# Performance work log

Hardware: AMD Instinct MI355X
Metric: run time of the kernel (lower is better)

The kernel has to match this reference:

```python
import jax, jax.numpy as jnp
import numpy as np

HID = 4096
HEADS = 32
HEAD_DIM = 128
SEQ = 2048
GROUP = 128          # AWQ quantization group size along the input (K) dim
QKV_OUT = 3 * HID
ROPE_BASE = 10000.0


def dequant(qweight, scales, zeros):
    # qweight: [K, N] int; scales/zeros: [K//GROUP, N]
    s = jnp.repeat(scales, GROUP, axis=0)
    z = jnp.repeat(zeros, GROUP, axis=0)
    return (qweight.astype(jnp.float32) - z) * s


def rotate_half(x):
    x1, x2 = jnp.split(x, 2, axis=-1)
    return jnp.concatenate((-x2, x1), axis=-1)


def setup_inputs() -> dict:
    key = jax.random.key(0)
    ks = jax.random.split(key, 8)
    hidden_states = jax.random.normal(ks[0], (1, SEQ, HID), dtype=jnp.float32)
    position_ids = jnp.arange(SEQ, dtype=jnp.int32)[None, :]
    qkv_qweight = jax.random.randint(ks[1], (HID, QKV_OUT), 0, 16, dtype=jnp.int32)
    qkv_scales = jax.random.uniform(ks[2], (HID // GROUP, QKV_OUT), dtype=jnp.float32) * 0.002
    qkv_zeros = jax.random.uniform(ks[3], (HID // GROUP, QKV_OUT), dtype=jnp.float32) * 16.0
    o_qweight = jax.random.randint(ks[4], (HID, HID), 0, 16, dtype=jnp.int32)
    o_scales = jax.random.uniform(ks[5], (HID // GROUP, HID), dtype=jnp.float32) * 0.002
    o_zeros = jax.random.uniform(ks[6], (HID // GROUP, HID), dtype=jnp.float32) * 16.0
    return {"hidden_states": hidden_states, "position_ids": position_ids,
            "qkv_qweight": qkv_qweight, "qkv_scales": qkv_scales, "qkv_zeros": qkv_zeros,
            "o_qweight": o_qweight, "o_scales": o_scales, "o_zeros": o_zeros}


def reference(hidden_states, position_ids, qkv_qweight, qkv_scales, qkv_zeros,
              o_qweight, o_scales, o_zeros):
    b, s, _ = hidden_states.shape
    # --- quantized QKV projection (dequant + GEMM) ---
    w_qkv = dequant(qkv_qweight, qkv_scales, qkv_zeros)        # [HID, 3*HID]
    proj = jnp.einsum('bsk,kn->bsn', hidden_states, w_qkv)     # [b, s, 3*HID]
    xqkv = proj.reshape(b, s, 3, HEADS, HEAD_DIM)
    # [b, h, s, d]
    q = jnp.transpose(xqkv[:, :, 0], (0, 2, 1, 3))
    k = jnp.transpose(xqkv[:, :, 1], (0, 2, 1, 3))
    v = jnp.transpose(xqkv[:, :, 2], (0, 2, 1, 3))
    # --- rotary embedding (no KV cache: kv_seq_len == s) ---
    inv_freq = 1.0 / (ROPE_BASE ** (jnp.arange(0, HEAD_DIM, 2, dtype=jnp.float32) / HEAD_DIM))
    t = jnp.arange(s, dtype=jnp.float32)
    freqs = jnp.outer(t, inv_freq)                             # [s, d/2]
    emb = jnp.concatenate((freqs, freqs), axis=-1)             # [s, d]
    cos = jnp.cos(emb)[position_ids][:, None]                  # [b, 1, s, d]
    sin = jnp.sin(emb)[position_ids][:, None]
    q = q * cos + rotate_half(q) * sin
    k = k * cos + rotate_half(k) * sin
    # --- causal attention (flash_attn_func, padding_mask=None branch) ---
    scale = 1.0 / jnp.sqrt(jnp.float32(HEAD_DIM))
    scores = jnp.einsum('bhqd,bhkd->bhqk', q, k) * scale       # [b, h, s, s]
    causal = jnp.tril(jnp.ones((s, s), dtype=bool))
    scores = jnp.where(causal, scores, jnp.float32(-1e30))
    probs = jax.nn.softmax(scores, axis=-1)
    attn = jnp.einsum('bhqk,bhkd->bhqd', probs, v)             # [b, h, s, d]
    attn = jnp.transpose(attn, (0, 2, 1, 3)).reshape(b, s, HID)
    # --- quantized output projection ---
    w_o = dequant(o_qweight, o_scales, o_zeros)                # [HID, HID]
    out = jnp.einsum('bsk,kn->bsn', attn, w_o)                 # [b, s, HID]
    return out
```

## Files before the change

### kernel.cpp

```cpp
#include <hip/hip_runtime.h>
#include <hip/hip_bf16.h>

#define S_LEN 2048
#define HID_DIM 4096
#define NH 32
#define HD 128
#define NQKV 12288

typedef _Float16 half2v __attribute__((ext_vector_type(2)));
typedef _Float16 half4v __attribute__((ext_vector_type(4)));
typedef _Float16 half8v __attribute__((ext_vector_type(8)));
typedef float f32x4 __attribute__((ext_vector_type(4)));

typedef const __attribute__((address_space(1))) unsigned int* gas_u32;
typedef __attribute__((address_space(3))) unsigned int* las_u32;

__device__ inline void g2lds16(const _Float16* g, _Float16* l) {
  __builtin_amdgcn_global_load_lds((gas_u32)g, (las_u32)l, 16, 0, 0);
}

__global__ __launch_bounds__(256) void dequant_w(const int* __restrict__ W,
                                                 const float* __restrict__ scal,
                                                 const float* __restrict__ zer,
                                                 _Float16* __restrict__ Wt, int K, int N) {
  __shared__ _Float16 lT[64 * 84];
  const int k0 = blockIdx.y * 64, n0 = blockIdx.x * 64;
  const int tid = threadIdx.x, c = tid & 63, rp = tid >> 6;
  const int g = k0 >> 7;
  const float sc = scal[(size_t)g * N + n0 + c];
  const float zp = zer[(size_t)g * N + n0 + c];
#pragma unroll
  for (int i = 0; i < 8; ++i) {
    const int k = i * 8 + rp * 2;
    const float q0 = (float)W[(size_t)(k0 + k) * N + n0 + c];
    const float q1 = (float)W[(size_t)(k0 + k + 1) * N + n0 + c];
    half2v p;
    p[0] = (_Float16)((q0 - zp) * sc);
    p[1] = (_Float16)((q1 - zp) * sc);
    *(half2v*)&lT[c * 84 + k] = p;
  }
  __syncthreads();
  const int kc = tid & 7, nr0 = tid >> 3;
#pragma unroll
  for (int i = 0; i < 2; ++i) {
    const int n = nr0 + 32 * i;
    union { half8v v8; half4v v4[2]; } u;
    u.v4[0] = *(const half4v*)&lT[n * 84 + kc * 8];
    u.v4[1] = *(const half4v*)&lT[n * 84 + kc * 8 + 4];
    *(half8v*)&Wt[(size_t)(n0 + n) * K + k0 + kc * 8] = u.v8;
  }
}

__global__ __launch_bounds__(256) void conv_a(const float* __restrict__ A, _Float16* __restrict__ Af) {
  const int i = blockIdx.x * 256 + threadIdx.x;
  const float4 t = ((const float4*)A)[i];
  half4v r;
  r[0] = (_Float16)t.x; r[1] = (_Float16)t.y; r[2] = (_Float16)t.z; r[3] = (_Float16)t.w;
  ((half4v*)Af)[i] = r;
}

__device__ inline void stage128x64(const _Float16* __restrict__ gp, int K,
                                   _Float16* lp, int wave, int stR, int stC) {
  g2lds16(gp + (size_t)(wave * 16 + stR) * K + stC, lp + (wave * 2) * 512);
  g2lds16(gp + (size_t)(wave * 16 + 8 + stR) * K + stC, lp + (wave * 2 + 1) * 512);
}
__device__ inline void stage64x64(const _Float16* __restrict__ gp, int K,
                                  _Float16* lp, int wave, int stR, int stC) {
  g2lds16(gp + (size_t)(wave * 8 + stR) * K + stC, lp + wave * 512);
}

template <int NBF, typename CT>
__global__ __launch_bounds__(512, 2) void gemm_2ph(const _Float16* __restrict__ A,
                                                   const _Float16* __restrict__ Bt,
                                                   CT* __restrict__ C, int M, int N, int K) {
  __shared__ _Float16 sA[3][2][128 * 64];
  __shared__ _Float16 sB[2][NBF * 64 * 64];

  const int tid = threadIdx.x;
  const int wave = tid >> 6, lane = tid & 63;
  const int quad = lane >> 4, l16 = lane & 15;
  const int wr = wave >> 2;
  const int wc = wave & 3;
  const int NT = K >> 6;

  const _Float16* Ab = A + (size_t)(blockIdx.y * 256) * K;
  const _Float16* Bb = Bt + (size_t)(blockIdx.x * (NBF * 64)) * K;

  const int stR = lane >> 3;
  const int stC = ((lane & 7) ^ stR) << 3;
  const int fx = l16 & 7;

#define COFF(ks_) ((((ks_) * 4 + quad) ^ fx) << 3)
#define SYNC_MFMA()                                  \
  __builtin_amdgcn_s_barrier();                      \
  asm volatile("s_waitcnt lgkmcnt(0)" ::: "memory"); \
  __builtin_amdgcn_sched_barrier(0);

  f32x4 acc[8][NBF];
  const f32x4 zero4 = {0.f, 0.f, 0.f, 0.f};
#pragma unroll
  for (int m8 = 0; m8 < 8; ++m8)
#pragma unroll
    for (int nb = 0; nb < NBF; ++nb) acc[m8][nb] = zero4;

#pragma unroll
  for (int j = 0; j < NBF; ++j)
    stage64x64(Bb + (size_t)(j * 64) * K, K, &sB[0][j * 4096], wave, stR, stC);
  stage128x64(Ab, K, &sA[0][0][0], wave, stR, stC);
  stage128x64(Ab + (size_t)128 * K, K, &sA[0][1][0], wave, stR, stC);
  stage128x64(Ab + 64, K, &sA[1][0][0], wave, stR, stC);
  stage128x64(Ab + (size_t)128 * K + 64, K, &sA[1][1][0], wave, stR, stC);
  asm volatile("s_waitcnt vmcnt(4)" ::: "memory");
  __builtin_amdgcn_s_barrier();

  int bA = 0;
  for (int t = 0; t < NT; ++t) {
    const int bB = t & 1;
    const int bA2 = (bA + 2 >= 3) ? bA - 1 : bA + 2;
    half8v af[4][2], bf[NBF][2];

#pragma unroll
    for (int mb = 0; mb < 4; ++mb)
#pragma unroll
      for (int ks = 0; ks < 2; ++ks)
        af[mb][ks] = *(const half8v*)&sA[bA][wr][(mb * 16 + l16) * 64 + COFF(ks)];
#pragma unroll
    for (int nb = 0; nb < NBF; ++nb)
#pragma unroll
      for (int ks = 0; ks < 2; ++ks)
        bf[nb][ks] = *(const half8v*)&sB[bB][(wc * (NBF * 16) + nb * 16 + l16) * 64 + COFF(ks)];
    if (t + 1 < NT) {
#pragma unroll
      for (int j = 0; j < NBF; ++j)
        stage64x64(Bb + (size_t)(j * 64) * K + (size_t)(t + 1) * 64, K,
                   &sB[bB ^ 1][j * 4096], wave, stR, stC);
    }
    SYNC_MFMA()
    __builtin_amdgcn_s_setprio(1);
#pragma unroll
    for (int mb = 0; mb < 4; ++mb)
#pragma unroll
      for (int nb = 0; nb < NBF; ++nb)
#pragma unroll
        for (int ks = 0; ks < 2; ++ks)
          acc[mb][nb] =
              __builtin_amdgcn_mfma_f32_16x16x32_f16(af[mb][ks], bf[nb][ks], acc[mb][nb], 0, 0, 0);
    __builtin_amdgcn_s_setprio(0);

#pragma unroll
    for (int mb = 0; mb < 4; ++mb)
#pragma unroll
      for (int ks = 0; ks < 2; ++ks)
        af[mb][ks] = *(const half8v*)&sA[bA][wr][(64 + mb * 16 + l16) * 64 + COFF(ks)];
    if (t + 2 < NT) {
      const _Float16* Ap = Ab + (size_t)(t + 2) * 64;
      stage128x64(Ap, K, &sA[bA2][0][0], wave, stR, stC);
      stage128x64(Ap + (size_t)128 * K, K, &sA[bA2][1][0], wave, stR, stC);
      asm volatile("s_waitcnt vmcnt(4)" ::: "memory");
    } else if (t + 1 < NT) {
      asm volatile("s_waitcnt vmcnt(0)" ::: "memory");
    }
    SYNC_MFMA()
    __builtin_amdgcn_s_setprio(1);
#pragma unroll
    for (int mb = 0; mb < 4; ++mb)
#pragma unroll
      for (int nb = 0; nb < NBF; ++nb)
#pragma unroll
        for (int ks = 0; ks < 2; ++ks)
          acc[4 + mb][nb] = __builtin_amdgcn_mfma_f32_16x16x32_f16(af[mb][ks], bf[nb][ks],
                                                                   acc[4 + mb][nb], 0, 0, 0);
    __builtin_amdgcn_s_setprio(0);

    bA = (bA + 1 >= 3) ? 0 : bA + 1;
  }

  const int rbase = blockIdx.y * 256 + wr * 128 + quad * 4;
  const int cbase = blockIdx.x * (NBF * 64) + wc * (NBF * 16) + l16;
#pragma unroll
  for (int m8 = 0; m8 < 8; ++m8) {
    const int rowb = rbase + (m8 >> 2) * 64 + (m8 & 3) * 16;
#pragma unroll
    for (int nb = 0; nb < NBF; ++nb)
#pragma unroll
      for (int i = 0; i < 4; ++i)
        C[(size_t)(rowb + i) * N + cbase + nb * 16] = (CT)acc[m8][nb][i];
  }
#undef COFF
#undef SYNC_MFMA
}

__global__ __launch_bounds__(256) void rope_kernel(const _Float16* __restrict__ proj,
                                                   const int* __restrict__ pos,
                                                   _Float16* __restrict__ Q, _Float16* __restrict__ K,
                                                   _Float16* __restrict__ Vt) {
  const int h = blockIdx.x, sb = blockIdx.y;
  const int tid = threadIdx.x;
  const int s0 = sb * 64;

#pragma unroll
  for (int it = 0; it < 16; ++it) {
    const int idx = it * 256 + tid;
    const int sl = idx >> 6, j = idx & 63;
    const int s = s0 + sl;
    const float p = (float)pos[s];
    const float invrev = exp2f(-0.20762050593045455f * (float)j) * 0.15915494309189535f;
    const float rev = p * invrev;
    const float frac = rev - floorf(rev);
    const float sn = __builtin_amdgcn_sinf(frac);
    const float cs = __builtin_amdgcn_cosf(frac);
    const _Float16* rp = proj + (size_t)s * NQKV + h * HD;
    {
      const float x1 = (float)rp[j], x2 = (float)rp[j + 64];
      _Float16* qp = Q + ((size_t)h * S_LEN + s) * HD;
      qp[j] = (_Float16)(x1 * cs - x2 * sn);
      qp[j + 64] = (_Float16)(x2 * cs + x1 * sn);
    }
    {
      const float x1 = (float)rp[HID_DIM + j], x2 = (float)rp[HID_DIM + j + 64];
      _Float16* kp = K + ((size_t)h * S_LEN + s) * HD;
      kp[j] = (_Float16)(x1 * cs - x2 * sn);
      kp[j + 64] = (_Float16)(x2 * cs + x1 * sn);
    }
  }

  __shared__ _Float16 lV[64 * 132];
#pragma unroll
  for (int r = 0; r < 4; ++r) {
    const int cid = r * 256 + tid;
    const int sl = cid >> 4;
    const int d0 = (cid & 15) * 8;
    const _Float16* vp = proj + (size_t)(s0 + sl) * NQKV + 2 * HID_DIM + h * HD + d0;
    *(half4v*)&lV[sl * 132 + d0] = *(const half4v*)vp;
    *(half4v*)&lV[sl * 132 + d0 + 4] = *(const half4v*)(vp + 4);
  }
  __syncthreads();
#pragma unroll
  for (int it = 0; it < 32; ++it) {
    const int d = it * 4 + (tid >> 6);
    const int sl = tid & 63;
    Vt[((size_t)h * HD + d) * S_LEN + s0 + sl] = lV[sl * 132 + d];
  }
}

__global__ __launch_bounds__(256) void flash_attn(const _Float16* __restrict__ Q,
                                                  const _Float16* __restrict__ Km,
                                                  const _Float16* __restrict__ Vt,
                                                  _Float16* __restrict__ O) {
  __shared__ _Float16 lK[4][32 * 128];
  __shared__ _Float16 lV[4][128 * 32];
  __shared__ _Float16 lP[4][2][16 * 40];
  const int h = blockIdx.y;
  const int xb = blockIdx.x;
  const int qb = (xb & 1) ? (15 - (xb >> 1)) : (xb >> 1);
  const int tid = threadIdx.x;
  const int wave = tid >> 6, lane = tid & 63;
  const int quad = lane >> 4, l16 = lane & 15;
  const int q0w = qb * 128 + wave * 32;
  const float scale = 0.08838834764831845f;

  const _Float16* Qh = Q + (size_t)h * S_LEN * HD;
  const _Float16* Kh = Km + (size_t)h * S_LEN * HD;
  const _Float16* Vh = Vt + (size_t)h * HD * S_LEN;

  const int kRow0 = wave * 8 + (lane >> 4);
  const int kSlot = lane & 15;
  const int vRow0 = wave * 32 + (lane >> 2);
  const int vSlot = lane & 3;

  auto stage_kv = [&](int kt_, int buf_) {
#pragma unroll
    for (int i = 0; i < 2; ++i) {
      const int row = kRow0 + i * 4;
      const int ck = kSlot ^ (row & 15);
      g2lds16(Kh + (size_t)(kt_ * 32 + row) * HD + ck * 8, &lK[buf_][(wave * 8 + i * 4) * 128]);
    }
#pragma unroll
    for (int i = 0; i < 2; ++i) {
      const int row = vRow0 + i * 16;
      const int cv = vSlot ^ ((row >> 1) & 3);
      g2lds16(Vh + (size_t)row * S_LEN + kt_ * 32 + cv * 8, &lV[buf_][(wave * 32 + i * 16) * 32]);
    }
  };

  half8v qf[2][4];
#pragma unroll
  for (int r = 0; r < 2; ++r)
#pragma unroll
    for (int c = 0; c < 4; ++c)
      qf[r][c] = *(const half8v*)&Qh[(size_t)(q0w + r * 16 + l16) * HD + c * 32 + quad * 8];

  const f32x4 zero4 = {0.f, 0.f, 0.f, 0.f};
  f32x4 o[2][8];
  f32x4 lp[2];
#pragma unroll
  for (int r = 0; r < 2; ++r) {
    lp[r] = zero4;
#pragma unroll
    for (int c = 0; c < 8; ++c) o[r][c] = zero4;
  }

  const int ntiles = 4 * qb + 4;
  stage_kv(0, 0);
  stage_kv(1, 1);

  for (int kt = 0; kt < ntiles; ++kt) {
    const int cb = kt & 3;
    if (kt + 2 < ntiles) {
      stage_kv(kt + 2, (kt + 2) & 3);
      asm volatile("s_waitcnt vmcnt(8)" ::: "memory");
    } else if (kt + 1 < ntiles) {
      asm volatile("s_waitcnt vmcnt(4)" ::: "memory");
    } else {
      asm volatile("s_waitcnt vmcnt(0)" ::: "memory");
    }
    __builtin_amdgcn_s_barrier();

    half8v kf[2][4];
#pragma unroll
    for (int hf = 0; hf < 2; ++hf)
#pragma unroll
      for (int c = 0; c < 4; ++c) {
        const int slot = (c * 4 + quad) ^ l16;
        kf[hf][c] = *(const half8v*)&lK[cb][(hf * 16 + l16) * 128 + slot * 8];
      }
    half8v vf[8];
#pragma unroll
    for (int c = 0; c < 8; ++c) {
      const int slot = quad ^ ((l16 >> 1) & 3);
      vf[c] = *(const half8v*)&lV[cb][(c * 16 + l16) * 32 + slot * 8];
    }

    f32x4 s[2][2];
#pragma unroll
    for (int r = 0; r < 2; ++r)
#pragma unroll
      for (int hf = 0; hf < 2; ++hf) {
        s[r][hf] = zero4;
#pragma unroll
        for (int c = 0; c < 4; ++c)
          s[r][hf] = __builtin_amdgcn_mfma_f32_16x16x32_f16(qf[r][c], kf[hf][c], s[r][hf], 0, 0, 0);
      }

#pragma unroll
    for (int r = 0; r < 2; ++r) {
      float p0[4], p1[4];
#pragma unroll
      for (int i = 0; i < 4; ++i) {
        const int row = q0w + r * 16 + quad * 4 + i;
        const int col0 = kt * 32 + l16, col1 = col0 + 16;
        const float e0 = __expf(s[r][0][i] * scale);
        const float e1 = __expf(s[r][1][i] * scale);
        p0[i] = (col0 <= row) ? e0 : 0.f;
        p1[i] = (col1 <= row) ? e1 : 0.f;
        lp[r][i] += p0[i] + p1[i];
      }
      _Float16* pw = lP[wave][r];
#pragma unroll
      for (int i = 0; i < 4; ++i) {
        pw[(quad * 4 + i) * 40 + l16] = (_Float16)p0[i];
        pw[(quad * 4 + i) * 40 + l16 + 16] = (_Float16)p1[i];
      }
    }
    half8v pa[2];
#pragma unroll
    for (int r = 0; r < 2; ++r) pa[r] = *(half8v*)&lP[wave][r][l16 * 40 + quad * 8];

#pragma unroll
    for (int c = 0; c < 8; ++c)
#pragma unroll
      for (int r = 0; r < 2; ++r)
        o[r][c] = __builtin_amdgcn_mfma_f32_16x16x32_f16(pa[r], vf[c], o[r][c], 0, 0, 0);
  }

#pragma unroll
  for (int r = 0; r < 2; ++r) {
    f32x4 ls = lp[r];
#pragma unroll
    for (int off = 1; off < 16; off <<= 1) {
#pragma unroll
      for (int i = 0; i < 4; ++i) ls[i] += __shfl_xor(ls[i], off);
    }
    f32x4 inv;
#pragma unroll
    for (int i = 0; i < 4; ++i) inv[i] = 1.f / ls[i];
#pragma unroll
    for (int c = 0; c < 8; ++c) {
#pragma unroll
      for (int i = 0; i < 4; ++i) {
        const int row = q0w + r * 16 + quad * 4 + i;
        O[(size_t)row * HID_DIM + h * HD + c * 16 + l16] = (_Float16)(o[r][c][i] * inv[i]);
      }
    }
  }
}

extern "C" void kernel_launch(void* const* d_in, const int* in_sizes, int n_in,
                              void* d_out, int out_size, void* d_ws, size_t ws_size,
                              hipStream_t stream) {
  const float* hidden = (const float*)d_in[0];
  const int* pos = (const int*)d_in[1];
  const int* qkv_w = (const int*)d_in[2];
  const float* qkv_s = (const float*)d_in[3];
  const float* qkv_z = (const float*)d_in[4];
  const int* o_w = (const int*)d_in[5];
  const float* o_s = (const float*)d_in[6];
  const float* o_z = (const float*)d_in[7];

  char* ws = (char*)d_ws;
  _Float16* Wt_qkv = (_Float16*)(ws + 0);
  _Float16* Qb = (_Float16*)(ws + 0);
  _Float16* Kb = (_Float16*)(ws + 16777216);
  _Float16* Vtb = (_Float16*)(ws + 33554432);
  _Float16* Af16 = (_Float16*)(ws + 100663296);
  _Float16* attn = (_Float16*)(ws + 100663296);
  _Float16* proj = (_Float16*)(ws + 117440512);
  _Float16* Wt_o = (_Float16*)(ws + 117440512);
  float* out = (float*)d_out;

  hipLaunchKernelGGL(dequant_w, dim3(192, 64), dim3(256), 0, stream,
                     qkv_w, qkv_s, qkv_z, Wt_qkv, 4096, 12288);
  hipLaunchKernelGGL(conv_a, dim3(8192), dim3(256), 0, stream, hidden, Af16);
  hipLaunchKernelGGL((gemm_2ph<3, _Float16>), dim3(64, 8), dim3(512), 0, stream,
                     Af16, Wt_qkv, proj, 2048, 12288, 4096);
  hipLaunchKernelGGL(rope_kernel, dim3(32, 32), dim3(256), 0, stream, proj, pos, Qb, Kb, Vtb);
  hipLaunchKernelGGL(dequant_w, dim3(64, 64), dim3(256), 0, stream,
                     o_w, o_s, o_z, Wt_o, 4096, 4096);
  hipLaunchKernelGGL(flash_attn, dim3(16, 32), dim3(256), 0, stream, Qb, Kb, Vtb, attn);
  hipLaunchKernelGGL((gemm_2ph<2, float>), dim3(32, 8), dim3(512), 0, stream,
                     attn, Wt_o, out, 2048, 4096, 4096);
}
```

Baseline: 719.3 us.

## Load K/V fragments directly from global memory in flash attention, dropping LDS staging

Result: slower. 853.0 us (+18.6%).

```diff
diff --git a/kernel.cpp b/kernel.cpp
--- a/kernel.cpp
+++ b/kernel.cpp
@@ -243,12 +243,10 @@
   }
 }
 
-__global__ __launch_bounds__(256) void flash_attn(const _Float16* __restrict__ Q,
-                                                  const _Float16* __restrict__ Km,
-                                                  const _Float16* __restrict__ Vt,
-                                                  _Float16* __restrict__ O) {
-  __shared__ _Float16 lK[4][32 * 128];
-  __shared__ _Float16 lV[4][128 * 32];
+__global__ __launch_bounds__(256, 2) void flash_attn(const _Float16* __restrict__ Q,
+                                                     const _Float16* __restrict__ Km,
+                                                     const _Float16* __restrict__ Vt,
+                                                     _Float16* __restrict__ O) {
   __shared__ _Float16 lP[4][2][16 * 40];
   const int h = blockIdx.y;
   const int xb = blockIdx.x;
@@ -263,26 +261,6 @@
   const _Float16* Kh = Km + (size_t)h * S_LEN * HD;
   const _Float16* Vh = Vt + (size_t)h * HD * S_LEN;
 
-  const int kRow0 = wave * 8 + (lane >> 4);
-  const int kSlot = lane & 15;
-  const int vRow0 = wave * 32 + (lane >> 2);
-  const int vSlot = lane & 3;
-
-  auto stage_kv = [&](int kt_, int buf_) {
-#pragma unroll
-    for (int i = 0; i < 2; ++i) {
-      const int row = kRow0 + i * 4;
-      const int ck = kSlot ^ (row & 15);
-      g2lds16(Kh + (size_t)(kt_ * 32 + row) * HD + ck * 8, &lK[buf_][(wave * 8 + i * 4) * 128]);
-    }
-#pragma unroll
-    for (int i = 0; i < 2; ++i) {
-      const int row = vRow0 + i * 16;
-      const int cv = vSlot ^ ((row >> 1) & 3);
-      g2lds16(Vh + (size_t)row * S_LEN + kt_ * 32 + cv * 8, &lV[buf_][(wave * 32 + i * 16) * 32]);
-    }
-  };
-
   half8v qf[2][4];
 #pragma unroll
   for (int r = 0; r < 2; ++r)
@@ -300,36 +278,21 @@
     for (int c = 0; c < 8; ++c) o[r][c] = zero4;
   }
 
+  const _Float16* kp = Kh + (size_t)l16 * HD + quad * 8;
+  const _Float16* vp = Vh + (size_t)l16 * S_LEN + quad * 8;
+
   const int ntiles = 4 * qb + 4;
-  stage_kv(0, 0);
-  stage_kv(1, 1);
-
   for (int kt = 0; kt < ntiles; ++kt) {
-    const int cb = kt & 3;
-    if (kt + 2 < ntiles) {
-      stage_kv(kt + 2, (kt + 2) & 3);
-      asm volatile("s_waitcnt vmcnt(8)" ::: "memory");
-    } else if (kt + 1 < ntiles) {
-      asm volatile("s_waitcnt vmcnt(4)" ::: "memory");
-    } else {
-      asm volatile("s_waitcnt vmcnt(0)" ::: "memory");
-    }
-    __builtin_amdgcn_s_barrier();
-
     half8v kf[2][4];
 #pragma unroll
     for (int hf = 0; hf < 2; ++hf)
 #pragma unroll
-      for (int c = 0; c < 4; ++c) {
-        const int slot = (c * 4 + quad) ^ l16;
-        kf[hf][c] = *(const half8v*)&lK[cb][(hf * 16 + l16) * 128 + slot * 8];
-      }
+      for (int c = 0; c < 4; ++c)
+        kf[hf][c] = *(const half8v*)(kp + (size_t)(kt * 32 + hf * 16) * HD + c * 32);
     half8v vf[8];
 #pragma unroll
-    for (int c = 0; c < 8; ++c) {
-      const int slot = quad ^ ((l16 >> 1) & 3);
-      vf[c] = *(const half8v*)&lV[cb][(c * 16 + l16) * 32 + slot * 8];
-    }
+    for (int c = 0; c < 8; ++c)
+      vf[c] = *(const half8v*)(vp + (size_t)(c * 16) * S_LEN + kt * 32);
 
     f32x4 s[2][2];
 #pragma unroll
```
